# Performance work log

Measured on AMD Instinct MI355X. Metric: run time of the kernel, lower is better.

## Reference

```python
import jax, jax.numpy as jnp
import numpy as np

VOCAB = 32000
EMB = 32
HID = 64
B = 1024
T = 512


def setup_inputs() -> dict:
    key = jax.random.key(0)
    ks = jax.random.split(key, 8)
    s_e = 1.0 / np.sqrt(EMB)
    s_h = 1.0 / np.sqrt(HID)
    return {
        "x": jax.random.randint(ks[0], (B, T), 0, VOCAB),
        "emb": jax.random.normal(ks[1], (VOCAB, EMB), jnp.float32),
        "W_ih": jax.random.uniform(ks[2], (4 * HID, EMB), jnp.float32, -s_h, s_h),
        "W_hh": jax.random.uniform(ks[3], (4 * HID, HID), jnp.float32, -s_h, s_h),
        "b_ih": jax.random.uniform(ks[4], (4 * HID,), jnp.float32, -s_h, s_h),
        "b_hh": jax.random.uniform(ks[5], (4 * HID,), jnp.float32, -s_h, s_h),
        "fc_W": jax.random.uniform(ks[6], (VOCAB, HID), jnp.float32, -s_h, s_h),
        "fc_b": jax.random.uniform(ks[7], (VOCAB,), jnp.float32, -s_h, s_h),
    }


def reference(x, emb, W_ih, W_hh, b_ih, b_hh, fc_W, fc_b):
    e = emb[x]  # [B, T, EMB]
    # Precompute input contribution to all gates for all timesteps: [B, T, 4H]
    xg = jnp.einsum("bte,ge->btg", e, W_ih) + b_ih + b_hh
    xg_t = jnp.transpose(xg, (1, 0, 2))  # [T, B, 4H] for scan over time

    def step(carry, xg_step):
        h, c = carry
        gates = xg_step + h @ W_hh.T  # [B, 4H]
        i, f, g, o = jnp.split(gates, 4, axis=-1)  # torch gate order i,f,g,o
        i = jax.nn.sigmoid(i)
        f = jax.nn.sigmoid(f)
        g = jnp.tanh(g)
        o = jax.nn.sigmoid(o)
        c = f * c + i * g
        h = o * jnp.tanh(c)
        return (h, c), None

    h0 = jnp.zeros((x.shape[0], HID), e.dtype)
    c0 = jnp.zeros((x.shape[0], HID), e.dtype)
    (h_last, _), _ = jax.lax.scan(step, (h0, c0), xg_t)
    # out[:, -1, :] of the LSTM is just the final hidden state
    return h_last @ fc_W.T + fc_b  # [B, VOCAB]
```

## Files before the change

kernel.cpp:

```cpp
#include <hip/hip_runtime.h>
#include <cstddef>
#include <cstdint>

#define VOCAB 32000
#define EMB 32
#define HID 64
#define NG 256
#define BATCH 1024
#define SEQ 512
#define NB 4
#define ROWB 72
#define PFD 8

#define L2E 1.44269504088896340736f

typedef short short8 __attribute__((ext_vector_type(8)));
typedef _Float16 half8 __attribute__((ext_vector_type(8)));
typedef float floatx4 __attribute__((ext_vector_type(4)));
typedef int int4v __attribute__((ext_vector_type(4)));

union FragH {
  half8 h;
  int4v v;
};

#define K1_ROWS 32
__global__ __launch_bounds__(256) void build_table(
    const float* __restrict__ emb, const float* __restrict__ W_ih,
    const float* __restrict__ b_ih, const float* __restrict__ b_hh,
    float* __restrict__ table) {
  __shared__ __align__(16) float erow[K1_ROWS * EMB];
  const int tid = threadIdx.x;
  const int v0 = blockIdx.x * K1_ROWS;
  const int gidx = (tid & 3) * 64 + (tid >> 2);
  const float sc = ((tid & 3) == 2) ? (2.0f * L2E) : (-L2E);

  float w[EMB];
#pragma unroll
  for (int e = 0; e < EMB; e += 4) {
    const float4 t = *(const float4*)&W_ih[gidx * EMB + e];
    w[e] = t.x; w[e + 1] = t.y; w[e + 2] = t.z; w[e + 3] = t.w;
  }
  const float bsum = b_ih[gidx] + b_hh[gidx];

  ((float4*)erow)[tid] = ((const float4*)&emb[(size_t)v0 * EMB])[tid];
  __syncthreads();

#pragma unroll 4
  for (int r = 0; r < K1_ROWS; ++r) {
    float acc = bsum;
#pragma unroll
    for (int e = 0; e < EMB; ++e) acc += erow[r * EMB + e] * w[e];
    table[(size_t)(v0 + r) * NG + tid] = acc * sc;
  }
}

__global__ __launch_bounds__(256) void lstm_mfma(
    const int* __restrict__ x, const float* __restrict__ table,
    const float* __restrict__ W_hh, float* __restrict__ h_out) {
  __shared__ __align__(16) _Float16 Hs[2][16 * ROWB];
  __shared__ int xls[NB * SEQ];

  const int tid = threadIdx.x;
  const int w = tid >> 6;
  const int lane = tid & 63;
  const int quad = lane >> 4;
  const int col = lane & 15;
  const int blk = blockIdx.x;
  const int myhid = w * 16 + col;

  {
    int* hz = (int*)&Hs[0][0];
    const int nz = (int)(sizeof(Hs) / 4);
    for (int i = tid; i < nz; i += 256) hz[i] = 0;
  }
  {
    const int* xsrc = &x[(size_t)blk * NB * SEQ];
    for (int i = tid; i < NB * SEQ; i += 256) xls[i] = xsrc[i] << 10;
  }

  FragH Bf[4][2];
#pragma unroll
  for (int ti = 0; ti < 4; ++ti) {
    const int n = (w + ti * 4) * 16 + col;
    const float sc = (ti == 2) ? (2.0f * L2E) : (-L2E);
#pragma unroll
    for (int ko = 0; ko < 2; ++ko) {
      const float* src = &W_hh[n * HID + ko * 32 + quad * 8];
#pragma unroll
      for (int j = 0; j < 8; ++j) Bf[ti][ko].h[j] = (_Float16)(src[j] * sc);
    }
  }

  float cs = 0.0f, hcur = 0.0f;

  __syncthreads();

  const int xrow = quad * SEQ;
  const char* __restrict__ tb4 = (const char*)(table + (size_t)myhid * 4);

  auto gather = [&](int tt) -> float4 {
    return *(const float4*)(tb4 + (size_t)(unsigned)xls[xrow + tt]);
  };

  float4 xg0 = gather(0), xg1 = gather(1), xg2 = gather(2), xg3 = gather(3);
  float4 xg4 = gather(4), xg5 = gather(5), xg6 = gather(6), xg7 = gather(7);

  auto step = [&](float4& XG, const int RB, const int TT) {
    const float xi = XG.x, xf = XG.y, xgg = XG.z, xo = XG.w;
    {
      const int tn = (TT + PFD < SEQ) ? TT + PFD : SEQ - 1;
      XG = gather(tn);
    }

    const int abase = col * ROWB + quad * 8;
    FragH A0, A1;
    A0.v = *(const int4v*)&Hs[RB][abase];
    A1.v = *(const int4v*)&Hs[RB][abase + 32];

    floatx4 g4[4];
#pragma unroll
    for (int ti = 0; ti < 4; ++ti) {
      floatx4 a = (floatx4){0.f, 0.f, 0.f, 0.f};
      a = __builtin_amdgcn_mfma_f32_16x16x32_f16(A0.h, Bf[ti][0].h, a, 0, 0, 0);
      a = __builtin_amdgcn_mfma_f32_16x16x32_f16(A1.h, Bf[ti][1].h, a, 0, 0, 0);
      g4[ti] = a;
    }

    {
      const float gi = __builtin_amdgcn_rcpf(1.0f + __builtin_amdgcn_exp2f(g4[0][0] + xi));
      const float gf = __builtin_amdgcn_rcpf(1.0f + __builtin_amdgcn_exp2f(g4[1][0] + xf));
      const float rg = __builtin_amdgcn_rcpf(1.0f + __builtin_amdgcn_exp2f(g4[2][0] + xgg));
      const float go = __builtin_amdgcn_rcpf(1.0f + __builtin_amdgcn_exp2f(g4[3][0] + xo));
      const float gg2 = fmaf(-4.0f * L2E, rg, 2.0f * L2E);
      cs = fmaf(gi, gg2, gf * cs);
      const float rc = __builtin_amdgcn_rcpf(1.0f + __builtin_amdgcn_exp2f(cs));
      hcur = go * fmaf(-2.0f, rc, 1.0f);
      Hs[RB ^ 1][(quad * 4) * ROWB + myhid] = (_Float16)hcur;
    }
    __syncthreads();
  };

  for (int t = 0; t < SEQ; t += 8) {
    step(xg0, 0, t);
    step(xg1, 1, t + 1);
    step(xg2, 0, t + 2);
    step(xg3, 1, t + 3);
    step(xg4, 0, t + 4);
    step(xg5, 1, t + 5);
    step(xg6, 0, t + 6);
    step(xg7, 1, t + 7);
  }

  h_out[((size_t)blk * NB + quad) * HID + myhid] = hcur;
}

#define FCV 128
__global__ __launch_bounds__(256, 1) void fc_mfma(
    const float* __restrict__ h, const float* __restrict__ fc_W,
    const float* __restrict__ fc_b, float* __restrict__ out) {
  const int tid = threadIdx.x;
  const int w = tid >> 6;
  const int lane = tid & 63;
  const int q = lane >> 4;
  const int c = lane & 15;
  const int nbase = blockIdx.x * FCV + w * 32;

  const floatx4 z4 = (floatx4){0.f, 0.f, 0.f, 0.f};

  FragH Bh[2][2], Bl[2][2];
#pragma unroll
  for (int nt = 0; nt < 2; ++nt) {
#pragma unroll
    for (int ko = 0; ko < 2; ++ko) {
      const float* src = &fc_W[(size_t)(nbase + nt * 16 + c) * HID + ko * 32 + q * 8];
#pragma unroll
      for (int j = 0; j < 8; ++j) {
        const float f = src[j];
        const _Float16 hi = (_Float16)f;
        Bh[nt][ko].h[j] = hi;
        Bl[nt][ko].h[j] = (_Float16)(f - (float)hi);
      }
    }
  }
  const float bias0 = fc_b[nbase + c];
  const float bias1 = fc_b[nbase + 16 + c];

  auto loadh = [&](int mc, floatx4& a0, floatx4& a1, floatx4& a2, floatx4& a3) {
    const float* hr = &h[(size_t)(mc * 16 + c) * HID + q * 8];
    a0 = *(const floatx4*)hr;
    a1 = *(const floatx4*)(hr + 4);
    a2 = *(const floatx4*)(hr + 32);
    a3 = *(const floatx4*)(hr + 36);
  };

  floatx4 p0, p1, p2, p3, n0, n1, n2, n3;
  loadh(0, p0, p1, p2, p3);

  for (int mc = 0; mc < BATCH / 16; ++mc) {
    if (mc + 1 < BATCH / 16) loadh(mc + 1, n0, n1, n2, n3);

    FragH Ah0, Al0, Ah1, Al1;
#pragma unroll
    for (int j = 0; j < 4; ++j) {
      float f = p0[j];
      _Float16 hi = (_Float16)f;
      Ah0.h[j] = hi; Al0.h[j] = (_Float16)(f - (float)hi);
      f = p1[j]; hi = (_Float16)f;
      Ah0.h[4 + j] = hi; Al0.h[4 + j] = (_Float16)(f - (float)hi);
      f = p2[j]; hi = (_Float16)f;
      Ah1.h[j] = hi; Al1.h[j] = (_Float16)(f - (float)hi);
      f = p3[j]; hi = (_Float16)f;
      Ah1.h[4 + j] = hi; Al1.h[4 + j] = (_Float16)(f - (float)hi);
    }

    floatx4 acc0 = __builtin_amdgcn_mfma_f32_16x16x32_f16(Ah0.h, Bh[0][0].h, z4, 0, 0, 0);
    floatx4 acc1 = __builtin_amdgcn_mfma_f32_16x16x32_f16(Ah0.h, Bh[1][0].h, z4, 0, 0, 0);
    acc0 = __builtin_amdgcn_mfma_f32_16x16x32_f16(Ah1.h, Bh[0][1].h, acc0, 0, 0, 0);
    acc1 = __builtin_amdgcn_mfma_f32_16x16x32_f16(Ah1.h, Bh[1][1].h, acc1, 0, 0, 0);
    acc0 = __builtin_amdgcn_mfma_f32_16x16x32_f16(Al0.h, Bh[0][0].h, acc0, 0, 0, 0);
    acc1 = __builtin_amdgcn_mfma_f32_16x16x32_f16(Al0.h, Bh[1][0].h, acc1, 0, 0, 0);
    acc0 = __builtin_amdgcn_mfma_f32_16x16x32_f16(Al1.h, Bh[0][1].h, acc0, 0, 0, 0);
    acc1 = __builtin_amdgcn_mfma_f32_16x16x32_f16(Al1.h, Bh[1][1].h, acc1, 0, 0, 0);
    acc0 = __builtin_amdgcn_mfma_f32_16x16x32_f16(Ah0.h, Bl[0][0].h, acc0, 0, 0, 0);
    acc1 = __builtin_amdgcn_mfma_f32_16x16x32_f16(Ah0.h, Bl[1][0].h, acc1, 0, 0, 0);
    acc0 = __builtin_amdgcn_mfma_f32_16x16x32_f16(Ah1.h, Bl[0][1].h, acc0, 0, 0, 0);
    acc1 = __builtin_amdgcn_mfma_f32_16x16x32_f16(Ah1.h, Bl[1][1].h, acc1, 0, 0, 0);

#pragma unroll
    for (int r = 0; r < 4; ++r) {
      const size_t row = (size_t)(mc * 16 + q * 4 + r) * VOCAB;
      __builtin_nontemporal_store(acc0[r] + bias0, &out[row + nbase + c]);
      __builtin_nontemporal_store(acc1[r] + bias1, &out[row + nbase + 16 + c]);
    }

    p0 = n0; p1 = n1; p2 = n2; p3 = n3;
  }
}

extern "C" void kernel_launch(void* const* d_in, const int* in_sizes, int n_in,
                              void* d_out, int out_size, void* d_ws, size_t ws_size,
                              hipStream_t stream) {
  const int* x = (const int*)d_in[0];
  const float* emb = (const float*)d_in[1];
  const float* W_ih = (const float*)d_in[2];
  const float* W_hh = (const float*)d_in[3];
  const float* b_ih = (const float*)d_in[4];
  const float* b_hh = (const float*)d_in[5];
  const float* fc_W = (const float*)d_in[6];
  const float* fc_b = (const float*)d_in[7];
  float* out = (float*)d_out;

  float* table = out;
  float* hbuf = (float*)d_ws;

  build_table<<<VOCAB / K1_ROWS, 256, 0, stream>>>(emb, W_ih, b_ih, b_hh, table);
  lstm_mfma<<<BATCH / NB, 256, 0, stream>>>(x, table, W_hh, hbuf);
  fc_mfma<<<VOCAB / FCV, 256, 0, stream>>>(hbuf, fc_W, fc_b, out);
}
```

Before: 315.9 us.

## Transpose FC MFMA operands for vector stores and split batch across grid y

```diff
diff --git a/kernel.cpp b/kernel.cpp
--- a/kernel.cpp
+++ b/kernel.cpp
@@ -165,10 +165,11 @@
   const int q = lane >> 4;
   const int c = lane & 15;
   const int nbase = blockIdx.x * FCV + w * 32;
+  const int mrow0 = blockIdx.y * (BATCH / 4);
 
   const floatx4 z4 = (floatx4){0.f, 0.f, 0.f, 0.f};
 
-  FragH Bh[2][2], Bl[2][2];
+  FragH Wh[2][2], Wl[2][2];
 #pragma unroll
   for (int nt = 0; nt < 2; ++nt) {
 #pragma unroll
@@ -178,16 +179,16 @@
       for (int j = 0; j < 8; ++j) {
         const float f = src[j];
         const _Float16 hi = (_Float16)f;
-        Bh[nt][ko].h[j] = hi;
-        Bl[nt][ko].h[j] = (_Float16)(f - (float)hi);
+        Wh[nt][ko].h[j] = hi;
+        Wl[nt][ko].h[j] = (_Float16)(f - (float)hi);
       }
     }
   }
-  const float bias0 = fc_b[nbase + c];
-  const float bias1 = fc_b[nbase + 16 + c];
+  const floatx4 bias0 = *(const floatx4*)&fc_b[nbase + q * 4];
+  const floatx4 bias1 = *(const floatx4*)&fc_b[nbase + 16 + q * 4];
 
   auto loadh = [&](int mc, floatx4& a0, floatx4& a1, floatx4& a2, floatx4& a3) {
-    const float* hr = &h[(size_t)(mc * 16 + c) * HID + q * 8];
+    const float* hr = &h[(size_t)(mrow0 + mc * 16 + c) * HID + q * 8];
     a0 = *(const floatx4*)hr;
     a1 = *(const floatx4*)(hr + 4);
     a2 = *(const floatx4*)(hr + 32);
@@ -197,41 +198,41 @@
   floatx4 p0, p1, p2, p3, n0, n1, n2, n3;
   loadh(0, p0, p1, p2, p3);
 
-  for (int mc = 0; mc < BATCH / 16; ++mc) {
-    if (mc + 1 < BATCH / 16) loadh(mc + 1, n0, n1, n2, n3);
-
-    FragH Ah0, Al0, Ah1, Al1;
+  const int NCH = BATCH / 4 / 16;
+  for (int mc = 0; mc < NCH; ++mc) {
+    if (mc + 1 < NCH) loadh(mc + 1, n0, n1, n2, n3);
+
+    FragH Hh0, Hl0, Hh1, Hl1;
 #pragma unroll
     for (int j = 0; j < 4; ++j) {
       float f = p0[j];
       _Float16 hi = (_Float16)f;
-      Ah0.h[j] = hi; Al0.h[j] = (_Float16)(f - (float)hi);
+      Hh0.h[j] = hi; Hl0.h[j] = (_Float16)(f - (float)hi);
       f = p1[j]; hi = (_Float16)f;
-      Ah0.h[4 + j] = hi; Al0.h[4 + j] = (_Float16)(f - (float)hi);
+      Hh0.h[4 + j] = hi; Hl0.h[4 + j] = (_Float16)(f - (float)hi);
       f = p2[j]; hi = (_Float16)f;
-      Ah1.h[j] = hi; Al1.h[j] = (_Float16)(f - (float)hi);
+      Hh1.h[j] = hi; Hl1.h[j] = (_Float16)(f - (float)hi);
       f = p3[j]; hi = (_Float16)f;
-      Ah1.h[4 + j] = hi; Al1.h[4 + j] = (_Float16)(f - (float)hi);
-    }
-
-    floatx4 acc0 = __builtin_amdgcn_mfma_f32_16x16x32_f16(Ah0.h, Bh[0][0].h, z4, 0, 0, 0);
-    floatx4 acc1 = __builtin_amdgcn_mfma_f32_16x16x32_f16(Ah0.h, Bh[1][0].h, z4, 0, 0, 0);
-    acc0 = __builtin_amdgcn_mfma_f32_16x16x32_f16(Ah1.h, Bh[0][1].h, acc0, 0, 0, 0);
-    acc1 = __builtin_amdgcn_mfma_f32_16x16x32_f16(Ah1.h, Bh[1][1].h, acc1, 0, 0, 0);
-    acc0 = __builtin_amdgcn_mfma_f32_16x16x32_f16(Al0.h, Bh[0][0].h, acc0, 0, 0, 0);
-    acc1 = __builtin_amdgcn_mfma_f32_16x16x32_f16(Al0.h, Bh[1][0].h, acc1, 0, 0, 0);
-    acc0 = __builtin_amdgcn_mfma_f32_16x16x32_f16(Al1.h, Bh[0][1].h, acc0, 0, 0, 0);
-    acc1 = __builtin_amdgcn_mfma_f32_16x16x32_f16(Al1.h, Bh[1][1].h, acc1, 0, 0, 0);
-    acc0 = __builtin_amdgcn_mfma_f32_16x16x32_f16(Ah0.h, Bl[0][0].h, acc0, 0, 0, 0);
-    acc1 = __builtin_amdgcn_mfma_f32_16x16x32_f16(Ah0.h, Bl[1][0].h, acc1, 0, 0, 0);
-    acc0 = __builtin_amdgcn_mfma_f32_16x16x32_f16(Ah1.h, Bl[0][1].h, acc0, 0, 0, 0);
-    acc1 = __builtin_amdgcn_mfma_f32_16x16x32_f16(Ah1.h, Bl[1][1].h, acc1, 0, 0, 0);
-
-#pragma unroll
-    for (int r = 0; r < 4; ++r) {
-      const size_t row = (size_t)(mc * 16 + q * 4 + r) * VOCAB;
-      __builtin_nontemporal_store(acc0[r] + bias0, &out[row + nbase + c]);
-      __builtin_nontemporal_store(acc1[r] + bias1, &out[row + nbase + 16 + c]);
+      Hh1.h[4 + j] = hi; Hl1.h[4 + j] = (_Float16)(f - (float)hi);
+    }
+
+    floatx4 acc0 = __builtin_amdgcn_mfma_f32_16x16x32_f16(Wh[0][0].h, Hh0.h, z4, 0, 0, 0);
+    floatx4 acc1 = __builtin_amdgcn_mfma_f32_16x16x32_f16(Wh[1][0].h, Hh0.h, z4, 0, 0, 0);
+    acc0 = __builtin_amdgcn_mfma_f32_16x16x32_f16(Wh[0][1].h, Hh1.h, acc0, 0, 0, 0);
+    acc1 = __builtin_amdgcn_mfma_f32_16x16x32_f16(Wh[1][1].h, Hh1.h, acc1, 0, 0, 0);
+    acc0 = __builtin_amdgcn_mfma_f32_16x16x32_f16(Wl[0][0].h, Hh0.h, acc0, 0, 0, 0);
+    acc1 = __builtin_amdgcn_mfma_f32_16x16x32_f16(Wl[1][0].h, Hh0.h, acc1, 0, 0, 0);
+    acc0 = __builtin_amdgcn_mfma_f32_16x16x32_f16(Wl[0][1].h, Hh1.h, acc0, 0, 0, 0);
+    acc1 = __builtin_amdgcn_mfma_f32_16x16x32_f16(Wl[1][1].h, Hh1.h, acc1, 0, 0, 0);
+    acc0 = __builtin_amdgcn_mfma_f32_16x16x32_f16(Wh[0][0].h, Hl0.h, acc0, 0, 0, 0);
+    acc1 = __builtin_amdgcn_mfma_f32_16x16x32_f16(Wh[1][0].h, Hl0.h, acc1, 0, 0, 0);
+    acc0 = __builtin_amdgcn_mfma_f32_16x16x32_f16(Wh[0][1].h, Hl1.h, acc0, 0, 0, 0);
+    acc1 = __builtin_amdgcn_mfma_f32_16x16x32_f16(Wh[1][1].h, Hl1.h, acc1, 0, 0, 0);
+
+    {
+      const size_t row = (size_t)(mrow0 + mc * 16 + c) * VOCAB;
+      __builtin_nontemporal_store(acc0 + bias0, (floatx4*)&out[row + nbase + q * 4]);
+      __builtin_nontemporal_store(acc1 + bias1, (floatx4*)&out[row + nbase + 16 + q * 4]);
     }
 
     p0 = n0; p1 = n1; p2 = n2; p3 = n3;
@@ -256,5 +257,6 @@
 
   build_table<<<VOCAB / K1_ROWS, 256, 0, stream>>>(emb, W_ih, b_ih, b_hh, table);
   lstm_mfma<<<BATCH / NB, 256, 0, stream>>>(x, table, W_hh, hbuf);
-  fc_mfma<<<VOCAB / FCV, 256, 0, stream>>>(hbuf, fc_W, fc_b, out);
-}
+  dim3 g3(VOCAB / FCV, 4);
+  fc_mfma<<<g3, 256, 0, stream>>>(hbuf, fc_W, fc_b, out);
+}
```

Result: no change. 321.2 us (+1.7%).
